# Kernel optimization log

Measured on AMD Instinct MI355X. Metric: run time of the kernel, lower is better.

Reference implementation:

```python
import jax, jax.numpy as jnp
import numpy as np

B, M = 512, 256
IN1, IN2, IN3 = 20000, 15000, 20000


def setup_inputs() -> dict:
    key = jax.random.key(0)
    ks = jax.random.split(key, 16)
    s1, s2, s3, s4 = 1.0 / np.sqrt(IN1), 1.0 / np.sqrt(IN2), 1.0 / np.sqrt(IN3), 1.0 / np.sqrt(4 * M)
    return {
        "expression": jax.random.normal(ks[0], (B, IN1), jnp.float32),
        "mutation": jax.random.uniform(ks[1], (B, IN2), jnp.float32),
        "cna": jax.random.normal(ks[2], (B, IN3), jnp.float32),
        "We_x": jax.random.normal(ks[3], (M, IN1), jnp.float32) * s1,
        "We_y": jax.random.normal(ks[4], (M, IN1), jnp.float32) * s1,
        "Wm_x": jax.random.normal(ks[5], (M, IN2), jnp.float32) * s2,
        "Wm_y": jax.random.normal(ks[6], (M, IN2), jnp.float32) * s2,
        "Wc_x": jax.random.normal(ks[7], (M, IN3), jnp.float32) * s3,
        "Wc_y": jax.random.normal(ks[8], (M, IN3), jnp.float32) * s3,
        "W3e": jax.random.normal(ks[9], (1, 4 * M), jnp.float32) * s4,
        "b3e": jnp.zeros((1,), jnp.float32),
        "W3m": jax.random.normal(ks[10], (1, 4 * M), jnp.float32) * s4,
        "b3m": jnp.zeros((1,), jnp.float32),
        "W3c": jax.random.normal(ks[11], (1, 4 * M), jnp.float32) * s4,
        "b3c": jnp.zeros((1,), jnp.float32),
    }


def reference(expression, mutation, cna, We_x, We_y, Wm_x, Wm_y, Wc_x, Wc_y,
              W3e, b3e, W3m, b3m, W3c, b3c):
    def proj(x, Wx, Wy):  # (B,F) -> (B,2,M)
        return jnp.stack([x @ Wx.T, x @ Wy.T], axis=1)

    def l2norm(t):  # normalize over the 2-row axis, like torch.norm(dim=1,keepdim=True)
        return t / jnp.linalg.norm(t, axis=1, keepdims=True)

    e = l2norm(proj(expression, We_x, We_y))
    m = l2norm(proj(mutation, Wm_x, Wm_y))
    c = l2norm(proj(cna, Wc_x, Wc_y))

    energy = lambda a, b: jnp.einsum('bkm,bkn->bmn', a, b)  # (B,M,M), k=2
    E_em, E_ec, E_mc = energy(e, m), energy(e, c), energy(m, c)

    att_em = jax.nn.softmax(E_em, axis=1)                     # softmax over dim1
    att_ec = jax.nn.softmax(E_ec, axis=1)
    att_me = jnp.swapaxes(jax.nn.softmax(E_em, axis=-1), 1, 2)
    att_mc = jax.nn.softmax(E_mc, axis=-1)                    # double permute cancels
    att_ce = jnp.swapaxes(jax.nn.softmax(E_ec, axis=-1), 1, 2)
    att_cm = jnp.swapaxes(jax.nn.softmax(E_mc, axis=-1), 1, 2)

    w = lambda x, a: jnp.einsum('bkm,bmn->bkn', x, a)  # (B,2,M)
    e_feat = jnp.concatenate([w(e, att_em), w(e, att_ec)], axis=1).reshape(-1, 4 * e.shape[-1])
    m_feat = jnp.concatenate([w(m, att_me), w(m, att_mc)], axis=1).reshape(-1, 4 * e.shape[-1])
    c_feat = jnp.concatenate([w(c, att_ce), w(c, att_cm)], axis=1).reshape(-1, 4 * e.shape[-1])

    head = lambda f, W, b: jnp.squeeze(jax.nn.sigmoid(f @ W.T + b))
    return head(e_feat, W3e, b3e), head(m_feat, W3m, b3m), head(c_feat, W3c, b3c)
```

## Files before the change

kernel.cpp:

```cpp
#include <hip/hip_runtime.h>
#include <hip/hip_bf16.h>

typedef short short8 __attribute__((ext_vector_type(8)));
typedef float float4v __attribute__((ext_vector_type(4)));

#define TK 32
#define MAXSPLIT 20
#define APAD 40

__device__ __forceinline__ unsigned int pack2bf(float a, float b) {
    unsigned int r;
    asm("v_cvt_pk_bf16_f32 %0, %1, %2" : "=v"(r) : "v"(a), "v"(b));
    return r;
}

__global__ __launch_bounds__(512, 2) void gemm_kernel(
    const float* __restrict__ Ae, const float* __restrict__ Am, const float* __restrict__ Ac,
    const float* __restrict__ Wex, const float* __restrict__ Wey,
    const float* __restrict__ Wmx, const float* __restrict__ Wmy,
    const float* __restrict__ Wcx, const float* __restrict__ Wcy,
    float* __restrict__ part, int* __restrict__ ctr, int nsplit)
{
    int nb = gridDim.x;
    int per = nb >> 3;
    __shared__ int sjob;
    if (threadIdx.x == 0) {
        unsigned xcd;
        asm volatile("s_getreg_b32 %0, hwreg(HW_REG_XCC_ID)" : "=s"(xcd));
        xcd &= 7;
        int j = 0;
        #pragma unroll 1
        for (int t = 0; t < 8; ++t) {
            int x = (xcd + t) & 7;
            int pos = atomicAdd(&ctr[x], 1);
            if (pos < per) { j = x * per + pos; break; }
        }
        sjob = j;
    }
    __syncthreads();
    int job = sjob;

    int mod = job / (4 * nsplit);
    int rem = job - mod * 4 * nsplit;
    int split = rem >> 2;
    int t2 = rem & 3;
    int ti = t2 >> 1, tj = t2 & 1;

    const float* A; const float* Wx; const float* Wy; int K;
    if (mod == 0)      { A = Ae; Wx = Wex; Wy = Wey; K = 20000; }
    else if (mod == 1) { A = Am; Wx = Wmx; Wy = Wmy; K = 15000; }
    else               { A = Ac; Wx = Wcx; Wy = Wcy; K = 20000; }

    int chunk = ((K + nsplit * TK - 1) / (nsplit * TK)) * TK;
    int kstart = split * chunk;
    int kend = kstart + chunk; if (kend > K) kend = K;
    if (kstart >= kend) return;
    int nstep = (kend - kstart + TK - 1) / TK;

    const float* Abase = A + (size_t)(ti * 256) * K;
    const float* Wbase = (tj == 0) ? Wx : Wy;

    __shared__ unsigned short As[2][256][APAD];
    __shared__ unsigned short Bs[2][256][APAD];

    int tid = threadIdx.x;
    int lane = tid & 63, w = tid >> 6;
    int wr = (w & 3) * 64;
    int wc = (w >> 2) * 128;
    int q = lane >> 4, r16 = lane & 15, q8 = q * 8;

    int ra0 = tid >> 3;
    int ca  = (tid & 7) * 4;

    float4v ar[4], br[4];
    auto loadAB = [&](int k0) {
        int k = k0 + ca; if (k > K - 4) k = K - 4;
        #pragma unroll
        for (int i = 0; i < 4; ++i) {
            ar[i] = *(const float4v*)(Abase + (size_t)(ra0 + i * 64) * K + k);
            br[i] = *(const float4v*)(Wbase + (size_t)(ra0 + i * 64) * K + k);
        }
    };
    auto storeAB = [&](int buf, int k0, bool tail) {
        bool kill = tail && (k0 + ca >= kend);
        #pragma unroll
        for (int i = 0; i < 4; ++i) {
            float4v va = ar[i], vb = br[i];
            if (kill) { va = (float4v){0.f,0.f,0.f,0.f}; vb = (float4v){0.f,0.f,0.f,0.f}; }
            uint2 pa, pb;
            pa.x = pack2bf(va[0], va[1]);
            pa.y = pack2bf(va[2], va[3]);
            pb.x = pack2bf(vb[0], vb[1]);
            pb.y = pack2bf(vb[2], vb[3]);
            *(uint2*)&As[buf][ra0 + i * 64][ca] = pa;
            *(uint2*)&Bs[buf][ra0 + i * 64][ca] = pb;
        }
    };

    float4v acc[4][8];
    #pragma unroll
    for (int a = 0; a < 4; ++a)
        #pragma unroll
        for (int b = 0; b < 8; ++b)
            acc[a][b] = (float4v){0.f, 0.f, 0.f, 0.f};

    auto computeStep = [&](int buf) {
        short8 fa[4], fb[8];
        #pragma unroll
        for (int a = 0; a < 4; ++a)
            fa[a] = *(const short8*)&As[buf][wr + a * 16 + r16][q8];
        #pragma unroll
        for (int b = 0; b < 8; ++b)
            fb[b] = *(const short8*)&Bs[buf][wc + b * 16 + r16][q8];
        #pragma unroll
        for (int a = 0; a < 4; ++a)
            #pragma unroll
            for (int b = 0; b < 8; ++b)
                acc[a][b] = __builtin_amdgcn_mfma_f32_16x16x32_bf16(fa[a], fb[b], acc[a][b], 0, 0, 0);
    };

    loadAB(kstart);
    storeAB(0, kstart, kstart + TK > kend);

    for (int s = 0; s < nstep; ++s) {
        int cur = s & 1;
        int k1 = kstart + (s + 1) * TK;
        bool more = (s + 1 < nstep);
        if (more) loadAB(k1);
        __syncthreads();
        computeStep(cur);
        if (more) storeAB(cur ^ 1, k1, k1 + TK > kend);
    }

    float* pbase = part + (size_t)((mod * 4 + t2) * nsplit + split) * 65536;
    #pragma unroll
    for (int a = 0; a < 4; ++a)
        #pragma unroll
        for (int b = 0; b < 8; ++b)
            #pragma unroll
            for (int r = 0; r < 4; ++r) {
                int row = wr + a * 16 + q * 4 + r;
                int col = wc + b * 16 + r16;
                pbase[row * 256 + col] = acc[a][b][r];
            }
}

__global__ void reduce_kernel(const float* __restrict__ part, float* __restrict__ P,
                              float* __restrict__ headacc, int nsplit)
{
    int gid = blockIdx.x * 256 + threadIdx.x;
    if (gid < 1536) headacc[gid] = 0.f;
    int mod = gid >> 18;
    int rem = gid & 262143;
    int b = rem >> 9, j = rem & 511;
    int ti = b >> 8, r = b & 255, tj = j >> 8, c = j & 255;
    int t2 = ti * 2 + tj;
    const float* src = part + (size_t)((mod * 4 + t2) * nsplit) * 65536 + r * 256 + c;
    float s = 0.f;
    for (int k = 0; k < nsplit; ++k) s += src[(size_t)k * 65536];
    P[gid] = s;
}

__global__ __launch_bounds__(256) void pairs_kernel(
    const float* __restrict__ P, float* __restrict__ headacc,
    const float* __restrict__ W3e, const float* __restrict__ W3m, const float* __restrict__ W3c)
{
    int b = blockIdx.x / 3, pair = blockIdx.x % 3;
    int t = threadIdx.x;
    __shared__ float2 Pn[256], Qn[256];
    __shared__ float Rinv[256];
    __shared__ float red[4];

    int pm = (pair == 2) ? 1 : 0;
    int qm = (pair == 0) ? 1 : 2;
    const float* prow = P + pm * 262144 + b * 512;
    const float* qrow = P + qm * 262144 + b * 512;

    float px = prow[t], py = prow[256 + t];
    float ip = rsqrtf(px * px + py * py);
    Pn[t] = (float2){px * ip, py * ip};
    float qx = qrow[t], qy = qrow[256 + t];
    float iq = rsqrtf(qx * qx + qy * qy);
    Qn[t] = (float2){qx * iq, qy * iq};
    __syncthreads();

    const float L2E = 1.4426950408889634f;

    float pxr = Pn[t].x * L2E, pyr = Pn[t].y * L2E;
    float rs = 0.f, rqx = 0.f, rqy = 0.f;
    #pragma unroll 4
    for (int j = 0; j < 256; ++j) {
        float2 qv = Qn[j];
        float x = exp2f(fmaf(pyr, qv.y, pxr * qv.x));
        rs += x;
        rqx = fmaf(qv.x, x, rqx);
        rqy = fmaf(qv.y, x, rqy);
    }
    float rinv = 1.f / rs;
    Rinv[t] = rinv;
    float Fq0 = rqx * rinv, Fq1 = rqy * rinv;

    const float* WR; int hR, offR;
    if (pair == 0)      { WR = W3m; hR = 1; offR = 0; }
    else if (pair == 1) { WR = W3c; hR = 2; offR = 0; }
    else                { WR = W3c; hR = 2; offR = 512; }
    float v = Fq0 * WR[offR + t] + Fq1 * WR[offR + 256 + t];
    #pragma unroll
    for (int o = 32; o > 0; o >>= 1) v += __shfl_down(v, o, 64);
    if ((t & 63) == 0) red[t >> 6] = v;
    __syncthreads();
    if (t == 0) atomicAdd(&headacc[b * 3 + hR], red[0] + red[1] + red[2] + red[3]);
    __syncthreads();

    float qxr = Qn[t].x * L2E, qyr = Qn[t].y * L2E;
    float cs = 0.f, cpx = 0.f, cpy = 0.f;
    if (pair < 2) {
        #pragma unroll 4
        for (int i = 0; i < 256; ++i) {
            float2 pv = Pn[i];
            float x = exp2f(fmaf(qyr, pv.y, qxr * pv.x));
            cs += x;
            cpx = fmaf(pv.x, x, cpx);
            cpy = fmaf(pv.y, x, cpy);
        }
        float ci = 1.f / cs;
        cpx *= ci; cpy *= ci;
    } else {
        #pragma unroll 4
        for (int i = 0; i < 256; ++i) {
            float2 pv = Pn[i];
            float x = exp2f(fmaf(qyr, pv.y, qxr * pv.x)) * Rinv[i];
            cpx = fmaf(pv.x, x, cpx);
            cpy = fmaf(pv.y, x, cpy);
        }
    }
    const float* WC; int hC, offC;
    if (pair == 0)      { WC = W3e; hC = 0; offC = 0; }
    else if (pair == 1) { WC = W3e; hC = 0; offC = 512; }
    else                { WC = W3m; hC = 1; offC = 512; }
    float v2 = cpx * WC[offC + t] + cpy * WC[offC + 256 + t];
    #pragma unroll
    for (int o = 32; o > 0; o >>= 1) v2 += __shfl_down(v2, o, 64);
    if ((t & 63) == 0) red[t >> 6] = v2;
    __syncthreads();
    if (t == 0) atomicAdd(&headacc[b * 3 + hC], red[0] + red[1] + red[2] + red[3]);
}

__global__ void head_kernel(const float* __restrict__ headacc,
                            const float* __restrict__ b3e, const float* __restrict__ b3m,
                            const float* __restrict__ b3c, float* __restrict__ out)
{
    int i = blockIdx.x * 256 + threadIdx.x;
    if (i >= 1536) return;
    int h = i >> 9, b = i & 511;
    float bias = (h == 0) ? b3e[0] : (h == 1) ? b3m[0] : b3c[0];
    float z = headacc[b * 3 + h] + bias;
    out[i] = 1.f / (1.f + __expf(-z));
}

extern "C" void kernel_launch(void* const* d_in, const int* in_sizes, int n_in,
                              void* d_out, int out_size, void* d_ws, size_t ws_size,
                              hipStream_t stream) {
    const float* Ae  = (const float*)d_in[0];
    const float* Am  = (const float*)d_in[1];
    const float* Ac  = (const float*)d_in[2];
    const float* Wex = (const float*)d_in[3];
    const float* Wey = (const float*)d_in[4];
    const float* Wmx = (const float*)d_in[5];
    const float* Wmy = (const float*)d_in[6];
    const float* Wcx = (const float*)d_in[7];
    const float* Wcy = (const float*)d_in[8];
    const float* W3e = (const float*)d_in[9];
    const float* b3e = (const float*)d_in[10];
    const float* W3m = (const float*)d_in[11];
    const float* b3m = (const float*)d_in[12];
    const float* W3c = (const float*)d_in[13];
    const float* b3c = (const float*)d_in[14];

    size_t fixed = (size_t)786432 * 4 + 1536 * 4 + 8 * 4;
    int nsplit = 2;
    if (ws_size > fixed) {
        size_t avail = (ws_size - fixed) / ((size_t)12 * 65536 * 4);
        nsplit = (avail < MAXSPLIT) ? (int)avail : MAXSPLIT;
        if (nsplit < 2) nsplit = 2;
    }
    nsplit &= ~1;

    float* part    = (float*)d_ws;
    float* P       = part + (size_t)12 * nsplit * 65536;
    float* headacc = P + 786432;
    int*   ctr     = (int*)(headacc + 1536);

    hipMemsetAsync(ctr, 0, 8 * sizeof(int), stream);
    gemm_kernel<<<12 * nsplit, 512, 0, stream>>>(Ae, Am, Ac, Wex, Wey, Wmx, Wmy, Wcx, Wcy,
                                                 part, ctr, nsplit);
    reduce_kernel<<<3072, 256, 0, stream>>>(part, P, headacc, nsplit);
    pairs_kernel<<<1536, 256, 0, stream>>>(P, headacc, W3e, W3m, W3c);
    head_kernel<<<6, 256, 0, stream>>>(headacc, b3e, b3m, b3c, (float*)d_out);
}
```

Before: 341.5 us.

## Double K tile to 64 and restructure global-to-LDS loading per row

Raises the K step from 32 to 64, so each step runs two MFMA sub-steps and the number of barriers and loop iterations per split halves. Global loads change from four rows with one float4 each per thread to one row with eight consecutive float4s per thread, and LDS writes become 128-bit stores. The A fragment is now loaded per row-tile inside the MFMA loop rather than all up front. In exchange, LDS use roughly doubles and staging registers (ar/br) double, which could hurt occupancy at launch_bounds(512,2), and each wave's global loads now cover fewer rows per instruction, which may change coalescing.

Result: slower. 414.7 us (+21.5%).

```diff
diff --git a/kernel.cpp b/kernel.cpp
--- a/kernel.cpp
+++ b/kernel.cpp
@@ -3,10 +3,11 @@
 
 typedef short short8 __attribute__((ext_vector_type(8)));
 typedef float float4v __attribute__((ext_vector_type(4)));
-
-#define TK 32
+typedef unsigned int uint4v __attribute__((ext_vector_type(4)));
+
+#define TK 64
 #define MAXSPLIT 20
-#define APAD 40
+#define WPAD 72
 
 __device__ __forceinline__ unsigned int pack2bf(float a, float b) {
     unsigned int r;
@@ -60,8 +61,8 @@
     const float* Abase = A + (size_t)(ti * 256) * K;
     const float* Wbase = (tj == 0) ? Wx : Wy;
 
-    __shared__ unsigned short As[2][256][APAD];
-    __shared__ unsigned short Bs[2][256][APAD];
+    __shared__ unsigned short As[2][256][WPAD];
+    __shared__ unsigned short Bs[2][256][WPAD];
 
     int tid = threadIdx.x;
     int lane = tid & 63, w = tid >> 6;
@@ -69,31 +70,39 @@
     int wc = (w >> 2) * 128;
     int q = lane >> 4, r16 = lane & 15, q8 = q * 8;
 
-    int ra0 = tid >> 3;
-    int ca  = (tid & 7) * 4;
-
-    float4v ar[4], br[4];
+    int row  = tid >> 1;
+    int half = (tid & 1) * 32;
+
+    float4v ar[8], br[8];
     auto loadAB = [&](int k0) {
-        int k = k0 + ca; if (k > K - 4) k = K - 4;
-        #pragma unroll
-        for (int i = 0; i < 4; ++i) {
-            ar[i] = *(const float4v*)(Abase + (size_t)(ra0 + i * 64) * K + k);
-            br[i] = *(const float4v*)(Wbase + (size_t)(ra0 + i * 64) * K + k);
+        int kb = k0 + half;
+        #pragma unroll
+        for (int j = 0; j < 8; ++j) {
+            int k = kb + j * 4; if (k > K - 4) k = K - 4;
+            ar[j] = *(const float4v*)(Abase + (size_t)row * K + k);
+            br[j] = *(const float4v*)(Wbase + (size_t)row * K + k);
         }
     };
     auto storeAB = [&](int buf, int k0, bool tail) {
-        bool kill = tail && (k0 + ca >= kend);
-        #pragma unroll
-        for (int i = 0; i < 4; ++i) {
-            float4v va = ar[i], vb = br[i];
-            if (kill) { va = (float4v){0.f,0.f,0.f,0.f}; vb = (float4v){0.f,0.f,0.f,0.f}; }
-            uint2 pa, pb;
-            pa.x = pack2bf(va[0], va[1]);
-            pa.y = pack2bf(va[2], va[3]);
-            pb.x = pack2bf(vb[0], vb[1]);
-            pb.y = pack2bf(vb[2], vb[3]);
-            *(uint2*)&As[buf][ra0 + i * 64][ca] = pa;
-            *(uint2*)&Bs[buf][ra0 + i * 64][ca] = pb;
+        unsigned int pa[16], pb[16];
+        #pragma unroll
+        for (int j = 0; j < 8; ++j) {
+            float4v va = ar[j], vb = br[j];
+            if (tail && (k0 + half + j * 4 >= kend)) {
+                va = (float4v){0.f,0.f,0.f,0.f};
+                vb = (float4v){0.f,0.f,0.f,0.f};
+            }
+            pa[2*j]   = pack2bf(va[0], va[1]);
+            pa[2*j+1] = pack2bf(va[2], va[3]);
+            pb[2*j]   = pack2bf(vb[0], vb[1]);
+            pb[2*j+1] = pack2bf(vb[2], vb[3]);
+        }
+        uint4v* dA = (uint4v*)&As[buf][row][half];
+        uint4v* dB = (uint4v*)&Bs[buf][row][half];
+        #pragma unroll
+        for (int j = 0; j < 4; ++j) {
+            dA[j] = (uint4v){pa[4*j], pa[4*j+1], pa[4*j+2], pa[4*j+3]};
+            dB[j] = (uint4v){pb[4*j], pb[4*j+1], pb[4*j+2], pb[4*j+3]};
         }
     };
 
@@ -105,18 +114,20 @@
             acc[a][b] = (float4v){0.f, 0.f, 0.f, 0.f};
 
     auto computeStep = [&](int buf) {
-        short8 fa[4], fb[8];
-        #pragma unroll
-        for (int a = 0; a < 4; ++a)
-            fa[a] = *(const short8*)&As[buf][wr + a * 16 + r16][q8];
-        #pragma unroll
-        for (int b = 0; b < 8; ++b)
-            fb[b] = *(const short8*)&Bs[buf][wc + b * 16 + r16][q8];
-        #pragma unroll
-        for (int a = 0; a < 4; ++a)
+        #pragma unroll
+        for (int kk = 0; kk < 2; ++kk) {
+            short8 fb[8];
             #pragma unroll
             for (int b = 0; b < 8; ++b)
-                acc[a][b] = __builtin_amdgcn_mfma_f32_16x16x32_bf16(fa[a], fb[b], acc[a][b], 0, 0, 0);
+                fb[b] = *(const short8*)&Bs[buf][wc + b * 16 + r16][kk * 32 + q8];
+            #pragma unroll
+            for (int a = 0; a < 4; ++a) {
+                short8 fa = *(const short8*)&As[buf][wr + a * 16 + r16][kk * 32 + q8];
+                #pragma unroll
+                for (int b = 0; b < 8; ++b)
+                    acc[a][b] = __builtin_amdgcn_mfma_f32_16x16x32_bf16(fa, fb[b], acc[a][b], 0, 0, 0);
+            }
+        }
     };
 
     loadAB(kstart);
@@ -139,9 +150,9 @@
         for (int b = 0; b < 8; ++b)
             #pragma unroll
             for (int r = 0; r < 4; ++r) {
-                int row = wr + a * 16 + q * 4 + r;
-                int col = wc + b * 16 + r16;
-                pbase[row * 256 + col] = acc[a][b][r];
+                int row2 = wr + a * 16 + q * 4 + r;
+                int col  = wc + b * 16 + r16;
+                pbase[row2 * 256 + col] = acc[a][b][r];
             }
 }
 
```
